# Kernel tuning notes

Hardware: AMD Instinct MI355X
Metric: run time of the kernel (lower is better)

## Reference

```python
import jax, jax.numpy as jnp
import numpy as np

B, N, F, T, K, O = 64, 34, 16, 96, 3, 64
EPS = 1e-8  # torch cosine_similarity eps


def _laplacian(A):
    # get_L_d: normalized graph Laplacian L = I - D^{-1/2} A D^{-1/2}
    n = A.shape[-1]
    d = A.sum(-1)                                   # (..., N) row-sum degrees
    dinv = jnp.where(d > 0, jax.lax.rsqrt(jnp.maximum(d, 1e-12)), 0.0)
    I = jnp.eye(n, dtype=A.dtype)
    return I - dinv[..., :, None] * A * dinv[..., None, :]


def _dynamic_adjacency(gs, position, distance):
    # gs: (B,T,N,F); uses features [1:3] as 2-d wind vector
    v = gs[..., 1:3]                                # (B,T,N,2)
    vn = jnp.linalg.norm(v, axis=-1)                # (B,T,N)
    pn = jnp.linalg.norm(position, axis=-1)         # (N,)
    dots = jnp.einsum('btnc,mc->btnm', v, position)  # (B,T,N,N)
    cos = dots / (jnp.maximum(vn, EPS)[..., None] * jnp.maximum(pn, EPS))
    cos = jnp.maximum(cos, 0.0)                     # cosine_sims[cos<=0]=0
    A = cos * vn[..., None] / distance              # wind_speed / distance
    # F.normalize(p=2, dim=(1,2)): per-sample Frobenius normalization
    frob = jnp.sqrt(jnp.sum(A * A, axis=(-2, -1), keepdims=True))
    return A / jnp.maximum(frob, 1e-12)


def setup_inputs() -> dict:
    key = jax.random.key(0)
    ks = jax.random.split(key, 6)
    x = jax.random.normal(ks[0], (B, N, F, T), jnp.float32)
    st_attention = jax.random.normal(ks[1], (B, K, N, N), jnp.float32)
    position = jax.random.normal(ks[2], (N, 2), jnp.float32)
    distance = jax.random.uniform(ks[3], (N, N), jnp.float32, 1.0, 10.0)
    Theta = jax.random.normal(ks[4], (K, F, O), jnp.float32) * 0.1
    Theta_L = jax.random.normal(ks[5], (K, F, O), jnp.float32) * 0.1
    return {"x": x, "st_attention": st_attention, "position": position,
            "distance": distance, "Theta": Theta, "Theta_L": Theta_L}


def reference(x, st_attention, position, distance, Theta, Theta_L):
    Kk = Theta.shape[0]
    gs = jnp.transpose(x, (0, 3, 1, 2))             # (B,T,N,F) -- vectorize over timesteps
    A = _dynamic_adjacency(gs, position, distance)  # (B,T,N,N)
    L1 = _laplacian(A)
    L2 = _laplacian(jnp.swapaxes(A, -1, -2))
    n = A.shape[-1]
    I = jnp.broadcast_to(jnp.eye(n, dtype=A.dtype), L1.shape)
    cheb1, cheb2 = [I, L1], [I, L2]
    for i in range(2, Kk):
        cheb1.append(2.0 * jnp.matmul(L1, cheb1[-1]) - cheb1[-2])
        cheb2.append(2.0 * jnp.matmul(L2, cheb2[-1]) - cheb2[-2])
    # softmax over dim=1 of (B,N,N) slice -> axis 2 of (B,K,N,N)
    att = jax.nn.softmax(st_attention, axis=2)      # (B,K,N,N)
    out = jnp.zeros(gs.shape[:3] + (Theta.shape[-1],), dtype=x.dtype)  # (B,T,N,O)
    for k in range(Kk):
        a = att[:, k][:, None]                       # (B,1,N,N) broadcast over T
        Tk1 = cheb1[k] * a
        Tk2 = cheb2[k] * a
        # T_k_with_att^T @ graph_signal @ theta
        out = out + jnp.einsum('btij,btif,fo->btjo', Tk1, gs, Theta[k]) \
                  + jnp.einsum('btij,btif,fo->btjo', Tk2, gs, Theta_L[k])
    out = jax.nn.relu(out)
    return jnp.transpose(out, (0, 2, 3, 1))          # (B,N,O,T)
```

## Files before the change

### kernel.cpp

```cpp
#include <hip/hip_runtime.h>
#include <cstddef>

namespace {
constexpr int cB = 64, cN = 34, cF = 16, cT = 96, cK = 3, cO = 64;
constexpr int LP = 72;
constexpr int BHP = 88;
constexpr int T4 = cT / 4;
constexpr float cEPS = 1e-8f;

typedef __attribute__((ext_vector_type(8))) _Float16 f16x8;
typedef __attribute__((ext_vector_type(8))) short   s16x8;
typedef __attribute__((ext_vector_type(4))) float   f32x4;

__device__ inline unsigned short f2h(float v) {
    _Float16 h = (_Float16)v;
    return __builtin_bit_cast(unsigned short, h);
}
__device__ inline float h2f(unsigned short u) {
    return (float)__builtin_bit_cast(_Float16, u);
}

__device__ inline size_t hstage_idx(int b, int t4, int j, int s) {
    return (((size_t)b * cN + j) * cO + (s >> 2)) * cT + 4 * t4 + (s & 3);
}
}

__global__ __launch_bounds__(256) void att_softmax_k(const float* __restrict__ st,
                                                     float* __restrict__ att) {
    int idx = blockIdx.x * blockDim.x + threadIdx.x;
    if (idx >= cB * cK * cN) return;
    int j = idx % cN;
    int bk = idx / cN;
    const float* base = st + (size_t)bk * cN * cN + j;
    float v[cN];
    float m = -3.402823466e38f;
#pragma unroll
    for (int i = 0; i < cN; ++i) { v[i] = base[(size_t)i * cN]; m = fmaxf(m, v[i]); }
    float s = 0.f;
#pragma unroll
    for (int i = 0; i < cN; ++i) { v[i] = __expf(v[i] - m); s += v[i]; }
    float inv = 1.f / s;
    float* ob = att + (size_t)bk * cN * cN + j;
#pragma unroll
    for (int i = 0; i < cN; ++i) ob[(size_t)i * cN] = v[i] * inv;
}

__global__ __launch_bounds__(256, 6) void cheb_h_k(
    const float* __restrict__ x,
    const float* __restrict__ att,
    const float* __restrict__ pos,
    const float* __restrict__ dist,
    unsigned* __restrict__ Hst)
{
    __shared__ __align__(16) unsigned short s_L1[cN * LP];
    __shared__ __align__(16) unsigned short s_L2[cN * LP];
    __shared__ __align__(16) unsigned short s_M1T[cN * LP];
    __shared__ __align__(16) unsigned short s_M3T[cN * LP];
    __shared__ __align__(16) unsigned short s_gsT[cF * LP];
    __shared__ float s_d0[cN], s_v1[cN], s_v2[cN], s_p1[cN], s_p2[cN], s_di1[cN], s_di2[cN];

    const int tid = threadIdx.x;
    const int lane = tid & 63;
    const int w = tid >> 6;
    const int lr = lane & 15;
    const int lg = lane >> 4;
    const int kb8 = lg * 8;

    const unsigned g = blockIdx.x;
    const unsigned lin = (g & 7u) * (cB * cT / 8) + (g >> 3);
    const int b = lin / cT, t = lin % cT;
    const int t4 = t >> 2, tt = t & 3;

    {
        f32x4 z = (f32x4){0.f, 0.f, 0.f, 0.f};
        for (int i2 = tid; i2 < cN * LP / 8; i2 += 256) {
            ((f32x4*)s_L1)[i2] = z; ((f32x4*)s_L2)[i2] = z;
            ((f32x4*)s_M1T)[i2] = z; ((f32x4*)s_M3T)[i2] = z;
        }
    }
    if (tid < cN) {
        float px = pos[2 * tid], py = pos[2 * tid + 1];
        float pn = sqrtf(px * px + py * py);
        float r = 1.f / fmaxf(pn, cEPS);
        s_p1[tid] = px * r; s_p2[tid] = py * r;
        s_d0[tid] = att[((size_t)b * cK) * cN * cN + tid * cN + tid];
    } else if (tid >= 64 && tid < 64 + cN) {
        int n = tid - 64;
        float x1 = x[(((size_t)b * cN + n) * cF + 1) * cT + t];
        float x2 = x[(((size_t)b * cN + n) * cF + 2) * cT + t];
        float vn = sqrtf(x1 * x1 + x2 * x2);
        float s = vn / fmaxf(vn, cEPS);
        s_v1[n] = x1 * s; s_v2[n] = x2 * s;
    }
    for (int idx = tid; idx < cF * LP; idx += 256) {
        int f = idx / LP, n = idx - f * LP;
        unsigned short v = 0;
        if (n < cN) v = f2h(x[(((size_t)b * cN + n) * cF + f) * cT + t]);
        s_gsT[idx] = v;
    }
    __syncthreads();

    float* Af = (float*)s_L1;
#pragma unroll
    for (int e = 0; e < 5; ++e) {
        int idx = tid + 256 * e;
        if (idx < cN * cN) {
            int i = idx / cN, m = idx - i * cN;
            float dot = s_v1[i] * s_p1[m] + s_v2[i] * s_p2[m];
            Af[idx] = __fdividef(fmaxf(dot, 0.f), dist[idx]);
        }
    }
    __syncthreads();

    if (tid < cN) {
        float s = 0.f;
#pragma unroll
        for (int m = 0; m < cN; ++m) s += Af[tid * cN + m];
        s_di1[tid] = (s > 0.f) ? rsqrtf(fmaxf(s, 1e-12f)) : 0.f;
    } else if (tid >= 64 && tid < 64 + cN) {
        int j = tid - 64;
        float s = 0.f;
#pragma unroll
        for (int i = 0; i < cN; ++i) s += Af[i * cN + j];
        s_di2[j] = (s > 0.f) ? rsqrtf(fmaxf(s, 1e-12f)) : 0.f;
    }
    float aij[5], aji[5];
#pragma unroll
    for (int e = 0; e < 5; ++e) {
        int idx = tid + 256 * e;
        if (idx < cN * cN) {
            int i = idx / cN, j = idx - i * cN;
            aij[e] = Af[idx];
            aji[e] = Af[j * cN + i];
        }
    }
    __syncthreads();

    const float* att1 = att + ((size_t)b * cK + 1) * cN * cN;
    const float* att2 = att + ((size_t)b * cK + 2) * cN * cN;
#pragma unroll
    for (int e = 0; e < 5; ++e) {
        int idx = tid + 256 * e;
        if (idx < cN * cN) {
            int i = idx / cN, j = idx - i * cN;
            float diag = (i == j) ? 1.f : 0.f;
            float l1 = diag - s_di1[i] * aij[e] * s_di1[j];
            float l2 = diag - s_di2[i] * aji[e] * s_di2[j];
            int rm = i * LP + j, tm = j * LP + i;
            s_L1[rm] = f2h(l1);
            s_L1[rm + cN] = 0;
            if (j < 4) s_L1[i * LP + 68 + j] = 0;
            s_L2[rm] = f2h(l2);
            float a1 = att1[idx];
            s_M1T[tm] = f2h(a1 * l1);
            s_M3T[tm] = f2h(a1 * l2);
        }
    }
    __syncthreads();

    const unsigned short* Ah = (w < 2) ? s_L1 : s_L2;
    const int nnt = (w & 1) ? 1 : 2;
    const int ntb0 = (w & 1) ? 32 : 0;
    f32x4 cd0[3], cd1[3];
#pragma unroll
    for (int mt = 0; mt < 3; ++mt) {
        cd0[mt] = (f32x4){0.f, 0.f, 0.f, 0.f};
        cd1[mt] = (f32x4){0.f, 0.f, 0.f, 0.f};
    }
#pragma unroll
    for (int ks = 0; ks < 2; ++ks) {
        f16x8 fah[3];
#pragma unroll
        for (int mt = 0; mt < 3; ++mt)
            fah[mt] = *(const f16x8*)&Ah[(mt * 16 + lr) * LP + 32 * ks + kb8];
#pragma unroll
        for (int un = 0; un < 2; ++un) {
            if (un == 1 && nnt < 2) break;
            int col = ntb0 + un * 16 + lr;
            s16x8 fbb;
#pragma unroll
            for (int e2 = 0; e2 < 8; ++e2) {
                int kk = 32 * ks + kb8 + e2;
                fbb[e2] = (kk < cN) ? (short)Ah[kk * LP + col] : (short)0;
            }
            f16x8 fb = __builtin_bit_cast(f16x8, fbb);
#pragma unroll
            for (int mt = 0; mt < 3; ++mt) {
                f32x4 acc = un ? cd1[mt] : cd0[mt];
                acc = __builtin_amdgcn_mfma_f32_16x16x32_f16(fah[mt], fb, acc, 0, 0, 0);
                if (un) cd1[mt] = acc; else cd0[mt] = acc;
            }
        }
    }
    __syncthreads();

    {
        unsigned short* Md = (w < 2) ? s_L1 : s_L2;
#pragma unroll
        for (int un = 0; un < 2; ++un) {
            if (un == 1 && nnt < 2) break;
            int jb = ntb0 + un * 16 + lr;
            if (jb < cN) {
#pragma unroll
                for (int mt = 0; mt < 3; ++mt) {
#pragma unroll
                    for (int h = 0; h < 2; ++h) {
                        int ia = mt * 16 + lg * 4 + 2 * h;
                        if (ia < cN) {
                            float dva = h ? (un ? cd1[mt][2] : cd0[mt][2])
                                          : (un ? cd1[mt][0] : cd0[mt][0]);
                            float dvb = h ? (un ? cd1[mt][3] : cd0[mt][3])
                                          : (un ? cd1[mt][1] : cd0[mt][1]);
                            float cva = 2.f * dva - ((ia == jb) ? 1.f : 0.f);
                            float cvb = 2.f * dvb - ((ia + 1 == jb) ? 1.f : 0.f);
                            unsigned lo = f2h(att2[ia * cN + jb] * cva);
                            unsigned hi = f2h(att2[(ia + 1) * cN + jb] * cvb);
                            ((unsigned*)Md)[(jb * LP + ia) >> 1] = lo | (hi << 16);
                        }
                    }
                }
            }
        }
    }
    __syncthreads();

    {
        const unsigned short* Ap = (w == 0) ? s_M1T : (w == 1) ? s_L1
                                 : (w == 2) ? s_M3T : s_L2;
        f32x4 hd[3];
#pragma unroll
        for (int mt = 0; mt < 3; ++mt) hd[mt] = (f32x4){0.f, 0.f, 0.f, 0.f};
#pragma unroll
        for (int ks = 0; ks < 2; ++ks) {
            f16x8 fb = *(const f16x8*)&s_gsT[lr * LP + 32 * ks + kb8];
#pragma unroll
            for (int mt = 0; mt < 3; ++mt) {
                f16x8 fa = *(const f16x8*)&Ap[(mt * 16 + lr) * LP + 32 * ks + kb8];
                hd[mt] = __builtin_amdgcn_mfma_f32_16x16x32_f16(fa, fb, hd[mt], 0, 0, 0);
            }
        }
        for (int idx = tid; idx < cN * 8; idx += 256) {
            int j = idx >> 3, c = idx & 7;
            float d = s_d0[j];
            unsigned lo = f2h(d * h2f(s_gsT[(2 * c) * LP + j]));
            unsigned hi = f2h(d * h2f(s_gsT[(2 * c + 1) * LP + j]));
            Hst[hstage_idx(b, t4, j, tt * 40 + c)] = lo | (hi << 16);
        }
        const int pc = 16 * (w + 1);
        const int cdw = (pc >> 1) + (lr >> 1);
#pragma unroll
        for (int mt = 0; mt < 3; ++mt) {
#pragma unroll
            for (int r = 0; r < 4; ++r) {
                int j = mt * 16 + lg * 4 + r;
                unsigned mine = (unsigned)f2h(hd[mt][r]);
                unsigned other = __shfl_xor(mine, 1, 64);
                unsigned dword = (lr & 1) ? ((other & 0xffffu) | (mine << 16))
                                          : (mine | (other << 16));
                bool mystore = ((lr & 1) == 0) ? (r < 2) : (r >= 2);
                if (mystore && j < cN)
                    Hst[hstage_idx(b, t4, j, tt * 40 + cdw)] = dword;
            }
        }
    }
}

__global__ __launch_bounds__(256, 4) void proj_k(
    const unsigned* __restrict__ Hst,
    const float* __restrict__ Th,
    const float* __restrict__ ThL,
    float* __restrict__ out)
{
    __shared__ __align__(16) unsigned short s_H[144 * BHP + 16];

    const int tid = threadIdx.x;
    const int lane = tid & 63;
    const int w = tid >> 6;
    const int lr = lane & 15;
    const int lg = lane >> 4;
    const int kb8 = lg * 8;
    const int ocol = w * 16 + lr;

    const unsigned g = blockIdx.x;
    const unsigned lin = (g & 7u) * (cB * T4 / 8) + (g >> 3);
    const int b = lin / T4, t4 = lin % T4;
    const int t0 = t4 * 4;

    f16x8 bfr[3];
#pragma unroll
    for (int s = 0; s < 3; ++s) {
#pragma unroll
        for (int j = 0; j < 8; ++j) {
            int cc = 32 * s + kb8 + j;
            float v = 0.f;
            if (cc < 80) {
                int p = cc >> 4, f = cc & 15;
                if (p == 0)      v = Th[f * cO + ocol] + ThL[f * cO + ocol];
                else if (p == 1) v = Th[(cF + f) * cO + ocol];
                else if (p == 2) v = Th[(2 * cF + f) * cO + ocol];
                else if (p == 3) v = ThL[(cF + f) * cO + ocol];
                else             v = ThL[(2 * cF + f) * cO + ocol];
            }
            bfr[s][j] = (_Float16)v;
        }
    }

    {
        unsigned* dst = (unsigned*)s_H;
        for (int i2 = tid; i2 < 144 * (BHP / 2); i2 += 256) {
            int r = i2 / (BHP / 2), c = i2 - r * (BHP / 2);
            unsigned v = 0u;
            if (r < 136 && c < 40) {
                int j = r >> 2, tt = r & 3;
                v = Hst[hstage_idx(b, t4, j, tt * 40 + c)];
            }
            dst[i2] = v;
        }
    }
    __syncthreads();

    f32x4 acc[9];
#pragma unroll
    for (int mt = 0; mt < 9; ++mt) acc[mt] = (f32x4){0.f, 0.f, 0.f, 0.f};
#pragma unroll
    for (int s = 0; s < 3; ++s) {
#pragma unroll
        for (int mt = 0; mt < 9; ++mt) {
            f16x8 a = *(const f16x8*)&s_H[(mt * 16 + lr) * BHP + kb8 + 32 * s];
            acc[mt] = __builtin_amdgcn_mfma_f32_16x16x32_f16(a, bfr[s], acc[mt], 0, 0, 0);
        }
    }

#pragma unroll
    for (int mt = 0; mt < 9; ++mt) {
        int j = 4 * mt + lg;
        if (j < cN) {
            float4 v;
            v.x = fmaxf(acc[mt][0], 0.f);
            v.y = fmaxf(acc[mt][1], 0.f);
            v.z = fmaxf(acc[mt][2], 0.f);
            v.w = fmaxf(acc[mt][3], 0.f);
            *(float4*)&out[(((size_t)b * cN + j) * cO + ocol) * cT + t0] = v;
        }
    }
}

extern "C" void kernel_launch(void* const* d_in, const int* in_sizes, int n_in,
                              void* d_out, int out_size, void* d_ws, size_t ws_size,
                              hipStream_t stream) {
    const float* x    = (const float*)d_in[0];
    const float* st   = (const float*)d_in[1];
    const float* pos  = (const float*)d_in[2];
    const float* dist = (const float*)d_in[3];
    const float* Th   = (const float*)d_in[4];
    const float* ThL  = (const float*)d_in[5];
    float* out = (float*)d_out;
    float* att = (float*)d_ws;
    unsigned* Hst = (unsigned*)d_out;

    att_softmax_k<<<(cB * cK * cN + 255) / 256, 256, 0, stream>>>(st, att);
    cheb_h_k<<<cB * cT, 256, 0, stream>>>(x, att, pos, dist, Hst);
    proj_k<<<cB * T4, 256, 0, stream>>>(Hst, Th, ThL, out);
}
```

Before: 90.96 us.

## Stage intermediate H in workspace with linear layout and prefetch attention/distance

When the workspace is large enough, the intermediate H tile is written to a separate workspace buffer in a contiguous per-(b,t4) layout, replacing the strided layout that reused the output buffer. This lets proj_k read its tile with coalesced contiguous loads. The cheb kernel also prefetches distance, att1 and att2 values into registers early so their global latency overlaps with setup. It splits the degree row and column sums across 136 threads using a shuffle reduction. The change depends on the workspace size, and the fallback keeps the old path.

```diff
diff --git a/kernel.cpp b/kernel.cpp
--- a/kernel.cpp
+++ b/kernel.cpp
@@ -7,6 +7,8 @@
 constexpr int BHP = 88;
 constexpr int T4 = cT / 4;
 constexpr float cEPS = 1e-8f;
+constexpr size_t WS_ATT = 1u << 20;
+constexpr size_t H_DW = (size_t)cB * T4 * 136 * 40;
 
 typedef __attribute__((ext_vector_type(8))) _Float16 f16x8;
 typedef __attribute__((ext_vector_type(8))) short   s16x8;
@@ -20,7 +22,10 @@
     return (float)__builtin_bit_cast(_Float16, u);
 }
 
-__device__ inline size_t hstage_idx(int b, int t4, int j, int s) {
+template <bool LIN>
+__device__ inline size_t hidx(int b, int t4, int j, int tt, int c) {
+    if (LIN) return ((size_t)(b * T4 + t4) * 136 + 4 * j + tt) * 40 + c;
+    int s = tt * 40 + c;
     return (((size_t)b * cN + j) * cO + (s >> 2)) * cT + 4 * t4 + (s & 3);
 }
 }
@@ -45,6 +50,7 @@
     for (int i = 0; i < cN; ++i) ob[(size_t)i * cN] = v[i] * inv;
 }
 
+template <bool LIN>
 __global__ __launch_bounds__(256, 6) void cheb_h_k(
     const float* __restrict__ x,
     const float* __restrict__ att,
@@ -71,6 +77,19 @@
     const int b = lin / cT, t = lin % cT;
     const int t4 = t >> 2, tt = t & 3;
 
+    const float* att1 = att + ((size_t)b * cK + 1) * cN * cN;
+    const float* att2 = att + ((size_t)b * cK + 2) * cN * cN;
+
+    float distr[5], a1r[5];
+#pragma unroll
+    for (int e = 0; e < 5; ++e) {
+        int idx = tid + 256 * e;
+        if (idx < cN * cN) {
+            distr[e] = dist[idx];
+            a1r[e] = att1[idx];
+        }
+    }
+
     {
         f32x4 z = (f32x4){0.f, 0.f, 0.f, 0.f};
         for (int i2 = tid; i2 < cN * LP / 8; i2 += 256) {
@@ -107,22 +126,29 @@
         if (idx < cN * cN) {
             int i = idx / cN, m = idx - i * cN;
             float dot = s_v1[i] * s_p1[m] + s_v2[i] * s_p2[m];
-            Af[idx] = __fdividef(fmaxf(dot, 0.f), dist[idx]);
-        }
-    }
-    __syncthreads();
-
-    if (tid < cN) {
-        float s = 0.f;
-#pragma unroll
-        for (int m = 0; m < cN; ++m) s += Af[tid * cN + m];
-        s_di1[tid] = (s > 0.f) ? rsqrtf(fmaxf(s, 1e-12f)) : 0.f;
-    } else if (tid >= 64 && tid < 64 + cN) {
-        int j = tid - 64;
-        float s = 0.f;
-#pragma unroll
-        for (int i = 0; i < cN; ++i) s += Af[i * cN + j];
-        s_di2[j] = (s > 0.f) ? rsqrtf(fmaxf(s, 1e-12f)) : 0.f;
+            Af[idx] = __fdividef(fmaxf(dot, 0.f), distr[e]);
+        }
+    }
+    __syncthreads();
+
+    if (tid < 136) {
+        int s = tid >> 1, half = tid & 1;
+        float acc = 0.f;
+        if (s < cN) {
+            const float* row = Af + s * cN + half * 17;
+#pragma unroll
+            for (int m = 0; m < 17; ++m) acc += row[m];
+        } else {
+            int j = s - cN;
+            const float* col = Af + half * 17 * cN + j;
+#pragma unroll
+            for (int i = 0; i < 17; ++i) acc += col[i * cN];
+        }
+        float tot = acc + __shfl_xor(acc, 1, 64);
+        if (half == 0) {
+            float d = (tot > 0.f) ? rsqrtf(fmaxf(tot, 1e-12f)) : 0.f;
+            if (s < cN) s_di1[s] = d; else s_di2[s - cN] = d;
+        }
     }
     float aij[5], aji[5];
 #pragma unroll
@@ -136,8 +162,6 @@
     }
     __syncthreads();
 
-    const float* att1 = att + ((size_t)b * cK + 1) * cN * cN;
-    const float* att2 = att + ((size_t)b * cK + 2) * cN * cN;
 #pragma unroll
     for (int e = 0; e < 5; ++e) {
         int idx = tid + 256 * e;
@@ -151,16 +175,36 @@
             s_L1[rm + cN] = 0;
             if (j < 4) s_L1[i * LP + 68 + j] = 0;
             s_L2[rm] = f2h(l2);
-            float a1 = att1[idx];
+            float a1 = a1r[e];
             s_M1T[tm] = f2h(a1 * l1);
             s_M3T[tm] = f2h(a1 * l2);
         }
     }
     __syncthreads();
 
-    const unsigned short* Ah = (w < 2) ? s_L1 : s_L2;
     const int nnt = (w & 1) ? 1 : 2;
     const int ntb0 = (w & 1) ? 32 : 0;
+    float a2r[2][3][2][2];
+#pragma unroll
+    for (int un = 0; un < 2; ++un) {
+        if (un == 1 && nnt < 2) break;
+        int jb = ntb0 + un * 16 + lr;
+        if (jb < cN) {
+#pragma unroll
+            for (int mt = 0; mt < 3; ++mt) {
+#pragma unroll
+                for (int h = 0; h < 2; ++h) {
+                    int ia = mt * 16 + lg * 4 + 2 * h;
+                    if (ia < cN) {
+                        a2r[un][mt][h][0] = att2[ia * cN + jb];
+                        a2r[un][mt][h][1] = att2[(ia + 1) * cN + jb];
+                    }
+                }
+            }
+        }
+    }
+
+    const unsigned short* Ah = (w < 2) ? s_L1 : s_L2;
     f32x4 cd0[3], cd1[3];
 #pragma unroll
     for (int mt = 0; mt < 3; ++mt) {
@@ -213,8 +257,8 @@
                                           : (un ? cd1[mt][1] : cd0[mt][1]);
                             float cva = 2.f * dva - ((ia == jb) ? 1.f : 0.f);
                             float cvb = 2.f * dvb - ((ia + 1 == jb) ? 1.f : 0.f);
-                            unsigned lo = f2h(att2[ia * cN + jb] * cva);
-                            unsigned hi = f2h(att2[(ia + 1) * cN + jb] * cvb);
+                            unsigned lo = f2h(a2r[un][mt][h][0] * cva);
+                            unsigned hi = f2h(a2r[un][mt][h][1] * cvb);
                             ((unsigned*)Md)[(jb * LP + ia) >> 1] = lo | (hi << 16);
                         }
                     }
@@ -244,7 +288,7 @@
             float d = s_d0[j];
             unsigned lo = f2h(d * h2f(s_gsT[(2 * c) * LP + j]));
             unsigned hi = f2h(d * h2f(s_gsT[(2 * c + 1) * LP + j]));
-            Hst[hstage_idx(b, t4, j, tt * 40 + c)] = lo | (hi << 16);
+            Hst[hidx<LIN>(b, t4, j, tt, c)] = lo | (hi << 16);
         }
         const int pc = 16 * (w + 1);
         const int cdw = (pc >> 1) + (lr >> 1);
@@ -259,12 +303,13 @@
                                           : (mine | (other << 16));
                 bool mystore = ((lr & 1) == 0) ? (r < 2) : (r >= 2);
                 if (mystore && j < cN)
-                    Hst[hstage_idx(b, t4, j, tt * 40 + cdw)] = dword;
-            }
-        }
-    }
-}
-
+                    Hst[hidx<LIN>(b, t4, j, tt, cdw)] = dword;
+            }
+        }
+    }
+}
+
+template <bool LIN>
 __global__ __launch_bounds__(256, 4) void proj_k(
     const unsigned* __restrict__ Hst,
     const float* __restrict__ Th,
@@ -311,8 +356,7 @@
             int r = i2 / (BHP / 2), c = i2 - r * (BHP / 2);
             unsigned v = 0u;
             if (r < 136 && c < 40) {
-                int j = r >> 2, tt = r & 3;
-                v = Hst[hstage_idx(b, t4, j, tt * 40 + c)];
+                v = Hst[hidx<LIN>(b, t4, r >> 2, r & 3, c)];
             }
             dst[i2] = v;
         }
@@ -356,9 +400,17 @@
     const float* ThL  = (const float*)d_in[5];
     float* out = (float*)d_out;
     float* att = (float*)d_ws;
-    unsigned* Hst = (unsigned*)d_out;
 
     att_softmax_k<<<(cB * cK * cN + 255) / 256, 256, 0, stream>>>(st, att);
-    cheb_h_k<<<cB * cT, 256, 0, stream>>>(x, att, pos, dist, Hst);
-    proj_k<<<cB * T4, 256, 0, stream>>>(Hst, Th, ThL, out);
-}
+
+    const bool use_ws = ws_size >= WS_ATT + H_DW * 4;
+    if (use_ws) {
+        unsigned* Hws = (unsigned*)((char*)d_ws + WS_ATT);
+        cheb_h_k<true><<<cB * cT, 256, 0, stream>>>(x, att, pos, dist, Hws);
+        proj_k<true><<<cB * T4, 256, 0, stream>>>(Hws, Th, ThL, out);
+    } else {
+        unsigned* Hst = (unsigned*)d_out;
+        cheb_h_k<false><<<cB * cT, 256, 0, stream>>>(x, att, pos, dist, Hst);
+        proj_k<false><<<cB * T4, 256, 0, stream>>>(Hst, Th, ThL, out);
+    }
+}
```

Measured after the change: 97.24 us. 6.9% more time.
